# Optimization experiments

Hardware: AMD Instinct MI355X
Metric: run time of the kernel (lower is better)

The kernel has to match this reference:

```python
import jax, jax.numpy as jnp
import numpy as np

B, S, E = 4, 2048, 1024
H, Dh = 16, 64


def setup_inputs() -> dict:
    key = jax.random.key(0)
    ks = jax.random.split(key, 9)
    scale_in = 1.0 / np.sqrt(E)
    scale_out = 1.0 / np.sqrt(H * Dh)
    x = jax.random.normal(ks[0], (B, S, E), dtype=jnp.float32)
    # Per-head projection weights stacked over heads: [H, E, Dh]
    Wq = jax.random.uniform(ks[1], (H, E, Dh), jnp.float32, -scale_in, scale_in)
    bq = jax.random.uniform(ks[2], (H, Dh), jnp.float32, -scale_in, scale_in)
    Wk = jax.random.uniform(ks[3], (H, E, Dh), jnp.float32, -scale_in, scale_in)
    bk = jax.random.uniform(ks[4], (H, Dh), jnp.float32, -scale_in, scale_in)
    Wv = jax.random.uniform(ks[5], (H, E, Dh), jnp.float32, -scale_in, scale_in)
    bv = jax.random.uniform(ks[6], (H, Dh), jnp.float32, -scale_in, scale_in)
    # Output projection: [H*Dh, E]
    Wo = jax.random.uniform(ks[7], (H * Dh, E), jnp.float32, -scale_out, scale_out)
    bo = jax.random.uniform(ks[8], (E,), jnp.float32, -scale_out, scale_out)
    return {"x": x, "Wq": Wq, "bq": bq, "Wk": Wk, "bk": bk,
            "Wv": Wv, "bv": bv, "Wo": Wo, "bo": bo}


def reference(x, Wq, bq, Wk, bk, Wv, bv, Wo, bo):
    # Per-head linear projections, batched over heads: [B, H, S, Dh]
    q = jnp.einsum('bse,hed->bhsd', x, Wq) + bq[None, :, None, :]
    k = jnp.einsum('bse,hed->bhsd', x, Wk) + bk[None, :, None, :]
    v = jnp.einsum('bse,hed->bhsd', x, Wv) + bv[None, :, None, :]
    scale = 1.0 / jnp.sqrt(jnp.asarray(Dh, dtype=x.dtype))
    scores = jnp.einsum('bhsd,bhtd->bhst', q, k) * scale  # [B, H, S, S]
    weights = jax.nn.softmax(scores, axis=-1)
    z = jnp.einsum('bhst,bhtd->bhsd', weights, v)  # [B, H, S, Dh]
    # Concat heads in module order: [B, S, H*Dh]
    z = jnp.transpose(z, (0, 2, 1, 3)).reshape(B, S, H * Dh)
    return z @ Wo + bo
```

## Files before the change

### kernel.cpp

```cpp
#include <hip/hip_runtime.h>
#include <hip/hip_bf16.h>

#define B_  4
#define S_  2048
#define E_  1024
#define H_  16
#define DH_ 64
#define M_  (B_*S_)
#define HD_ (H_*DH_)

typedef unsigned short u16;
typedef __attribute__((ext_vector_type(8))) __bf16 bf16x8;
typedef __attribute__((ext_vector_type(4))) __bf16 bf16x4;
typedef __attribute__((ext_vector_type(4))) float  f32x4;

#if __has_builtin(__builtin_amdgcn_exp2f)
#define EXP2F __builtin_amdgcn_exp2f
#else
#define EXP2F __builtin_exp2f
#endif

#define QSCALE 0.18033688011112042f

__device__ __forceinline__ void g2l16(const void* g, void* l) {
  __builtin_amdgcn_global_load_lds(
      (const __attribute__((address_space(1))) void*)g,
      (__attribute__((address_space(3))) void*)l, 16, 0, 0);
}

__device__ __forceinline__ u16 f2bf(float f) {
  union { float f; unsigned u; } v; v.f = f;
  unsigned r = v.u + 0x7FFFu + ((v.u >> 16) & 1u);
  return (u16)(r >> 16);
}

__global__ __launch_bounds__(256) void cvt_x_kernel(const float* __restrict__ x,
                                                    u16* __restrict__ xb) {
  int i = blockIdx.x * 256 + threadIdx.x;
  float4 v = ((const float4*)x)[i];
  ushort4 o;
  o.x = f2bf(v.x); o.y = f2bf(v.y); o.z = f2bf(v.z); o.w = f2bf(v.w);
  ((ushort4*)xb)[i] = o;
}

__global__ __launch_bounds__(256) void pack_wqkv_kernel(
    const float* __restrict__ Wq, const float* __restrict__ Wk,
    const float* __restrict__ Wv, u16* __restrict__ wt) {
  __shared__ u16 tile[64][66];
  int p = blockIdx.z, h = blockIdx.y, e0 = blockIdx.x * 64;
  const float* src = (p == 0 ? Wq : (p == 1 ? Wk : Wv)) + h * (E_ * DH_);
  int tid = threadIdx.x;
#pragma unroll
  for (int r = 0; r < 16; ++r) {
    int idx = r * 256 + tid;
    int el = idx >> 6, d = idx & 63;
    tile[el][d] = f2bf(src[(e0 + el) * DH_ + d]);
  }
  __syncthreads();
  u16* dst = wt + (p * HD_ + h * DH_) * E_;
#pragma unroll
  for (int r = 0; r < 16; ++r) {
    int idx = r * 256 + tid;
    int d = idx >> 6, el = idx & 63;
    dst[d * E_ + e0 + el] = tile[el][d];
  }
}

__global__ __launch_bounds__(256) void pack_wo_kernel(const float* __restrict__ Wo,
                                                      u16* __restrict__ wt) {
  __shared__ u16 tile[64][66];
  int c0 = blockIdx.y * 64, e0 = blockIdx.x * 64;
  int tid = threadIdx.x;
#pragma unroll
  for (int r = 0; r < 16; ++r) {
    int idx = r * 256 + tid;
    int cl = idx >> 6, el = idx & 63;
    tile[cl][el] = f2bf(Wo[(c0 + cl) * E_ + e0 + el]);
  }
  __syncthreads();
#pragma unroll
  for (int r = 0; r < 16; ++r) {
    int idx = r * 256 + tid;
    int er = idx >> 6, cl = idx & 63;
    wt[(e0 + er) * HD_ + c0 + cl] = tile[cl][er];
  }
}

__global__ __launch_bounds__(256) void transpose_v_kernel(
    const u16* __restrict__ vin, u16* __restrict__ vout) {
  __shared__ u16 t[64][72];
  const int tid = threadIdx.x;
  const int bh = blockIdx.y, st = blockIdx.x * 64;
  const u16* src = vin + ((size_t)((bh >> 4) * S_ + st)) * HD_ + (bh & 15) * 64;
#pragma unroll
  for (int rr = 0; rr < 2; ++rr) {
    int idx = rr * 256 + tid;
    int s = idx >> 3, ch = idx & 7;
    *(uint4*)&t[s][ch * 8] = *(const uint4*)(src + s * HD_ + ch * 8);
  }
  __syncthreads();
  u16* dst = vout + ((size_t)bh) * DH_ * S_ + st;
#pragma unroll
  for (int rr = 0; rr < 2; ++rr) {
    int idx = rr * 256 + tid;
    int d = idx >> 3, sc = (idx & 7) * 8;
    ushort4 o0, o1;
    o0.x = t[sc + 0][d]; o0.y = t[sc + 1][d]; o0.z = t[sc + 2][d]; o0.w = t[sc + 3][d];
    o1.x = t[sc + 4][d]; o1.y = t[sc + 5][d]; o1.z = t[sc + 6][d]; o1.w = t[sc + 7][d];
    *(ushort4*)(dst + (size_t)d * S_ + sc) = o0;
    *(ushort4*)(dst + (size_t)d * S_ + sc + 4) = o1;
  }
}

template <int MODE>
__global__ __launch_bounds__(256) void gemm_bt_kernel(
    const u16* __restrict__ A, const u16* __restrict__ Bt,
    const float* __restrict__ b0, const float* __restrict__ b1,
    const float* __restrict__ b2,
    u16* __restrict__ oQ, u16* __restrict__ oK, u16* __restrict__ oV,
    float* __restrict__ oF) {
  constexpr int K = 1024;
  __shared__ __align__(16) u16 As[128 * 32];
  __shared__ __align__(16) u16 Bs[128 * 32];
  const int tid = threadIdx.x;
  const int lane = tid & 63, wv = tid >> 6;
  const int wm = (wv >> 1) * 64, wn = (wv & 1) * 64;
  const int q4 = lane >> 4, lm = lane & 15;
  const int tileM = blockIdx.y * 128, tileN = blockIdx.x * 128;

  const int c0 = tid, c1 = tid + 256;
  const u16* gA0 = A + (tileM + (c0 >> 2)) * K + (((c0 & 3) ^ ((c0 >> 2) & 3)) * 8);
  const u16* gA1 = A + (tileM + (c1 >> 2)) * K + (((c1 & 3) ^ ((c1 >> 2) & 3)) * 8);
  const u16* gB0 = Bt + (tileN + (c0 >> 2)) * K + (((c0 & 3) ^ ((c0 >> 2) & 3)) * 8);
  const u16* gB1 = Bt + (tileN + (c1 >> 2)) * K + (((c1 & 3) ^ ((c1 >> 2) & 3)) * 8);
  u16* lA0 = As + c0 * 8; u16* lA1 = As + c1 * 8;
  u16* lB0 = Bs + c0 * 8; u16* lB1 = Bs + c1 * 8;

  f32x4 acc[4][4] = {};

  int aoff[4], boff[4];
#pragma unroll
  for (int i = 0; i < 4; ++i) {
    int ra = wm + i * 16 + lm;
    aoff[i] = ra * 32 + ((q4 ^ (ra & 3)) * 8);
    int rb = wn + i * 16 + lm;
    boff[i] = rb * 32 + ((q4 ^ (rb & 3)) * 8);
  }

  for (int k0 = 0; k0 < K; k0 += 32) {
    g2l16(gA0 + k0, lA0);
    g2l16(gA1 + k0, lA1);
    g2l16(gB0 + k0, lB0);
    g2l16(gB1 + k0, lB1);
    __syncthreads();
    bf16x8 af[4], bf[4];
#pragma unroll
    for (int i = 0; i < 4; ++i) af[i] = *(const bf16x8*)(As + aoff[i]);
#pragma unroll
    for (int j = 0; j < 4; ++j) bf[j] = *(const bf16x8*)(Bs + boff[j]);
#pragma unroll
    for (int i = 0; i < 4; ++i)
#pragma unroll
      for (int j = 0; j < 4; ++j)
        acc[i][j] = __builtin_amdgcn_mfma_f32_16x16x32_bf16(af[i], bf[j], acc[i][j], 0, 0, 0);
    __syncthreads();
  }

#pragma unroll
  for (int j = 0; j < 4; ++j) {
    int n = tileN + wn + j * 16 + lm;
    float bs;
    int proj = 0, cc = n;
    if (MODE == 1) {
      bs = b0[n];
    } else {
      proj = n >> 10; cc = n & 1023;
      const float* bp = (proj == 0 ? b0 : (proj == 1 ? b1 : b2));
      bs = bp[cc];
    }
#pragma unroll
    for (int i = 0; i < 4; ++i) {
#pragma unroll
      for (int r = 0; r < 4; ++r) {
        int m = tileM + wm + i * 16 + q4 * 4 + r;
        float val = acc[i][j][r] + bs;
        if (MODE == 1) {
          oF[m * HD_ + n] = val;
        } else {
          u16* optr = (proj == 0 ? oQ : (proj == 1 ? oK : oV));
          float scl = (proj == 0 ? QSCALE : 1.0f);
          optr[m * 1024 + cc] = f2bf(val * scl);
        }
      }
    }
  }
}

__global__ __launch_bounds__(256, 2) void flash_kernel(
    const u16* __restrict__ Q, const u16* __restrict__ Kb,
    const u16* __restrict__ Vt, u16* __restrict__ Z) {
  __shared__ __align__(16) u16 Ks[2][64 * 64];
  __shared__ __align__(16) u16 Vs[2][64 * 64];
  const int tid = threadIdx.x, lane = tid & 63, wv = tid >> 6;
  const int q4 = lane >> 4, lm = lane & 15;

  const int bid = blockIdx.x;
  const int bh = bid >> 3, qt = bid & 7;
  const int b = bh >> 4, h = bh & 15;

  const u16* qbase = Q + ((size_t)(b * S_ + qt * 256)) * HD_ + h * DH_;
  const u16* kbase = Kb + (size_t)b * S_ * HD_ + h * DH_;
  const u16* vbase = Vt + ((size_t)(b * H_ + h)) * DH_ * S_;
  u16* zbase = Z + ((size_t)(b * S_ + qt * 256)) * HD_ + h * DH_;

  const int c0 = tid,       r0 = c0 >> 3, s0 = ((c0 & 7) ^ (r0 & 7)) * 8;
  const int c1 = tid + 256, r1 = c1 >> 3, s1 = ((c1 & 7) ^ (r1 & 7)) * 8;
  const int kr0 = ((r0 >> 4) & 1) * 32 + ((r0 >> 2) & 3) * 8 + (r0 >> 5) * 4 + (r0 & 3);
  const int kr1 = ((r1 >> 4) & 1) * 32 + ((r1 >> 2) & 3) * 8 + (r1 >> 5) * 4 + (r1 & 3);

  bf16x8 qf[4][2];
#pragma unroll
  for (int qs = 0; qs < 4; ++qs)
#pragma unroll
    for (int dc = 0; dc < 2; ++dc)
      qf[qs][dc] = *(const bf16x8*)(qbase + (wv * 64 + qs * 16 + lm) * HD_ + dc * 32 + q4 * 8);

  const bf16x8 ones = {(__bf16)1.f, (__bf16)1.f, (__bf16)1.f, (__bf16)1.f,
                       (__bf16)1.f, (__bf16)1.f, (__bf16)1.f, (__bf16)1.f};

  int koff[4][2], voff[2][4];
#pragma unroll
  for (int kb = 0; kb < 4; ++kb)
#pragma unroll
    for (int dc = 0; dc < 2; ++dc) {
      int row = kb * 16 + lm;
      koff[kb][dc] = row * 64 + (((dc * 4 + q4) ^ (row & 7)) * 8);
    }
#pragma unroll
  for (int ck = 0; ck < 2; ++ck)
#pragma unroll
    for (int db = 0; db < 4; ++db) {
      int row = db * 16 + lm;
      voff[ck][db] = row * 64 + (((ck * 4 + q4) ^ (row & 7)) * 8);
    }

  f32x4 oacc[4][4] = {};
  f32x4 liacc[4] = {};

  {
    g2l16(kbase + kr0 * HD_ + s0, Ks[0] + c0 * 8);
    g2l16(kbase + kr1 * HD_ + s1, Ks[0] + c1 * 8);
    g2l16(vbase + r0 * S_ + s0, Vs[0] + c0 * 8);
    g2l16(vbase + r1 * S_ + s1, Vs[0] + c1 * 8);
  }

  for (int t = 0; t < 32; ++t) {
    const int pb = t & 1;
    __syncthreads();
    if (t < 31) {
      const u16* kt = kbase + (size_t)(t + 1) * 64 * HD_;
      const u16* vt = vbase + (t + 1) * 64;
      g2l16(kt + kr0 * HD_ + s0, Ks[1 - pb] + c0 * 8);
      g2l16(kt + kr1 * HD_ + s1, Ks[1 - pb] + c1 * 8);
      g2l16(vt + r0 * S_ + s0, Vs[1 - pb] + c0 * 8);
      g2l16(vt + r1 * S_ + s1, Vs[1 - pb] + c1 * 8);
    }
    const u16* Kp = Ks[pb];
    const u16* Vp = Vs[pb];

#pragma unroll
    for (int ck = 0; ck < 2; ++ck) {
      bf16x8 ka0 = *(const bf16x8*)(Kp + koff[ck][0]);
      bf16x8 ka1 = *(const bf16x8*)(Kp + koff[ck][1]);
      bf16x8 kb0 = *(const bf16x8*)(Kp + koff[ck + 2][0]);
      bf16x8 kb1 = *(const bf16x8*)(Kp + koff[ck + 2][1]);
      bf16x8 pf[4];
#pragma unroll
      for (int qs = 0; qs < 4; ++qs) {
        f32x4 sa = {}, sb = {};
        sa = __builtin_amdgcn_mfma_f32_16x16x32_bf16(ka0, qf[qs][0], sa, 0, 0, 0);
        sa = __builtin_amdgcn_mfma_f32_16x16x32_bf16(ka1, qf[qs][1], sa, 0, 0, 0);
        sb = __builtin_amdgcn_mfma_f32_16x16x32_bf16(kb0, qf[qs][0], sb, 0, 0, 0);
        sb = __builtin_amdgcn_mfma_f32_16x16x32_bf16(kb1, qf[qs][1], sb, 0, 0, 0);
        f32x4 pa, pb2;
#pragma unroll
        for (int r = 0; r < 4; ++r) { pa[r] = EXP2F(sa[r]); pb2[r] = EXP2F(sb[r]); }
        bf16x4 la = __builtin_convertvector(pa, bf16x4);
        bf16x4 lb = __builtin_convertvector(pb2, bf16x4);
        pf[qs] = __builtin_shufflevector(la, lb, 0, 1, 2, 3, 4, 5, 6, 7);
      }
#pragma unroll
      for (int qs = 0; qs < 4; ++qs)
        liacc[qs] = __builtin_amdgcn_mfma_f32_16x16x32_bf16(pf[qs], ones, liacc[qs], 0, 0, 0);
#pragma unroll
      for (int db = 0; db < 4; ++db) {
        bf16x8 vf = *(const bf16x8*)(Vp + voff[ck][db]);
#pragma unroll
        for (int qs = 0; qs < 4; ++qs)
          oacc[qs][db] = __builtin_amdgcn_mfma_f32_16x16x32_bf16(pf[qs], vf, oacc[qs][db], 0, 0, 0);
      }
    }
  }

#pragma unroll
  for (int qs = 0; qs < 4; ++qs) {
    float rin[4];
#pragma unroll
    for (int r = 0; r < 4; ++r) rin[r] = 1.f / liacc[qs][r];
#pragma unroll
    for (int db = 0; db < 4; ++db)
#pragma unroll
      for (int r = 0; r < 4; ++r)
        zbase[(wv * 64 + qs * 16 + q4 * 4 + r) * HD_ + db * 16 + lm] =
            f2bf(oacc[qs][db][r] * rin[r]);
  }
}

extern "C" void kernel_launch(void* const* d_in, const int* in_sizes, int n_in,
                              void* d_out, int out_size, void* d_ws, size_t ws_size,
                              hipStream_t stream) {
  const float* x  = (const float*)d_in[0];
  const float* Wq = (const float*)d_in[1];
  const float* bq = (const float*)d_in[2];
  const float* Wk = (const float*)d_in[3];
  const float* bk = (const float*)d_in[4];
  const float* Wv = (const float*)d_in[5];
  const float* bv = (const float*)d_in[6];
  const float* Wo = (const float*)d_in[7];
  const float* bo = (const float*)d_in[8];
  float* out = (float*)d_out;

  char* w = (char*)d_ws;
  u16*   xb    = (u16*)w;   w += (size_t)M_ * E_ * 2;
  u16*   wqkvT = (u16*)w;   w += (size_t)3 * HD_ * E_ * 2;
  u16*   woT   = (u16*)w;   w += (size_t)E_ * HD_ * 2;
  u16*   qB    = (u16*)w;   w += (size_t)M_ * HD_ * 2;
  u16*   kB    = (u16*)w;   w += (size_t)M_ * HD_ * 2;
  u16*   vT    = (u16*)w;   w += (size_t)M_ * HD_ * 2;
  u16*   zB    = (u16*)w;   w += (size_t)M_ * HD_ * 2;
  u16*   vB    = zB;

  cvt_x_kernel<<<dim3(M_ * E_ / 4 / 256), 256, 0, stream>>>(x, xb);
  pack_wqkv_kernel<<<dim3(16, 16, 3), 256, 0, stream>>>(Wq, Wk, Wv, wqkvT);
  pack_wo_kernel<<<dim3(16, 16), 256, 0, stream>>>(Wo, woT);
  gemm_bt_kernel<0><<<dim3(24, 64), 256, 0, stream>>>(xb, wqkvT, bq, bk, bv,
                                                      qB, kB, vB, nullptr);
  transpose_v_kernel<<<dim3(32, 64), 256, 0, stream>>>(vB, vT);
  flash_kernel<<<dim3(512), 256, 0, stream>>>(qB, kB, vT, zB);
  gemm_bt_kernel<1><<<dim3(8, 64), 256, 0, stream>>>(zB, woT, bo, nullptr, nullptr,
                                                     nullptr, nullptr, nullptr, out);
}
```

Before: 284.1 us.

## Merge prep kernels, deepen GEMM K-tile to 64, use vector bf16 conversion in epilogues

Fuses the x conversion and the two weight-packing kernels into one launch that dispatches on block index, removing two kernel launches. The GEMM's K-tile grows from 32 to 64 with an 8-way XOR swizzle, halving the number of barrier pairs per tile at the cost of double the LDS footprint. The GEMM and flash epilogues replace the manual round-to-nearest bf16 conversion with a vector convertvector, though the stores are still scattered 16-bit writes.

```diff
diff --git a/kernel.cpp b/kernel.cpp
--- a/kernel.cpp
+++ b/kernel.cpp
@@ -34,55 +34,53 @@
   return (u16)(r >> 16);
 }
 
-__global__ __launch_bounds__(256) void cvt_x_kernel(const float* __restrict__ x,
-                                                    u16* __restrict__ xb) {
-  int i = blockIdx.x * 256 + threadIdx.x;
-  float4 v = ((const float4*)x)[i];
-  ushort4 o;
-  o.x = f2bf(v.x); o.y = f2bf(v.y); o.z = f2bf(v.z); o.w = f2bf(v.w);
-  ((ushort4*)xb)[i] = o;
-}
-
-__global__ __launch_bounds__(256) void pack_wqkv_kernel(
-    const float* __restrict__ Wq, const float* __restrict__ Wk,
-    const float* __restrict__ Wv, u16* __restrict__ wt) {
+__global__ __launch_bounds__(256) void prep_kernel(
+    const float* __restrict__ x, const float* __restrict__ Wq,
+    const float* __restrict__ Wk, const float* __restrict__ Wv,
+    const float* __restrict__ Wo,
+    u16* __restrict__ xb, u16* __restrict__ wqkvT, u16* __restrict__ woT) {
   __shared__ u16 tile[64][66];
-  int p = blockIdx.z, h = blockIdx.y, e0 = blockIdx.x * 64;
-  const float* src = (p == 0 ? Wq : (p == 1 ? Wk : Wv)) + h * (E_ * DH_);
-  int tid = threadIdx.x;
-#pragma unroll
-  for (int r = 0; r < 16; ++r) {
-    int idx = r * 256 + tid;
-    int el = idx >> 6, d = idx & 63;
-    tile[el][d] = f2bf(src[(e0 + el) * DH_ + d]);
-  }
-  __syncthreads();
-  u16* dst = wt + (p * HD_ + h * DH_) * E_;
-#pragma unroll
-  for (int r = 0; r < 16; ++r) {
-    int idx = r * 256 + tid;
-    int d = idx >> 6, el = idx & 63;
-    dst[d * E_ + e0 + el] = tile[el][d];
-  }
-}
-
-__global__ __launch_bounds__(256) void pack_wo_kernel(const float* __restrict__ Wo,
-                                                      u16* __restrict__ wt) {
-  __shared__ u16 tile[64][66];
-  int c0 = blockIdx.y * 64, e0 = blockIdx.x * 64;
-  int tid = threadIdx.x;
-#pragma unroll
-  for (int r = 0; r < 16; ++r) {
-    int idx = r * 256 + tid;
-    int cl = idx >> 6, el = idx & 63;
-    tile[cl][el] = f2bf(Wo[(c0 + cl) * E_ + e0 + el]);
-  }
-  __syncthreads();
-#pragma unroll
-  for (int r = 0; r < 16; ++r) {
-    int idx = r * 256 + tid;
-    int er = idx >> 6, cl = idx & 63;
-    wt[(e0 + er) * HD_ + c0 + cl] = tile[cl][er];
+  const int blk = blockIdx.x, tid = threadIdx.x;
+  if (blk < 8192) {
+    int i = blk * 256 + tid;
+    float4 v = ((const float4*)x)[i];
+    ushort4 o;
+    o.x = f2bf(v.x); o.y = f2bf(v.y); o.z = f2bf(v.z); o.w = f2bf(v.w);
+    ((ushort4*)xb)[i] = o;
+  } else if (blk < 8960) {
+    int b2 = blk - 8192;
+    int p = b2 >> 8, h = (b2 >> 4) & 15, e0 = (b2 & 15) * 64;
+    const float* src = (p == 0 ? Wq : (p == 1 ? Wk : Wv)) + h * (E_ * DH_);
+#pragma unroll
+    for (int r = 0; r < 16; ++r) {
+      int idx = r * 256 + tid;
+      int el = idx >> 6, d = idx & 63;
+      tile[el][d] = f2bf(src[(e0 + el) * DH_ + d]);
+    }
+    __syncthreads();
+    u16* dst = wqkvT + (p * HD_ + h * DH_) * E_;
+#pragma unroll
+    for (int r = 0; r < 16; ++r) {
+      int idx = r * 256 + tid;
+      int d = idx >> 6, el = idx & 63;
+      dst[d * E_ + e0 + el] = tile[el][d];
+    }
+  } else {
+    int b3 = blk - 8960;
+    int c0 = (b3 >> 4) * 64, e0 = (b3 & 15) * 64;
+#pragma unroll
+    for (int r = 0; r < 16; ++r) {
+      int idx = r * 256 + tid;
+      int cl = idx >> 6, el = idx & 63;
+      tile[cl][el] = f2bf(Wo[(c0 + cl) * E_ + e0 + el]);
+    }
+    __syncthreads();
+#pragma unroll
+    for (int r = 0; r < 16; ++r) {
+      int idx = r * 256 + tid;
+      int er = idx >> 6, cl = idx & 63;
+      woT[(e0 + er) * HD_ + c0 + cl] = tile[cl][er];
+    }
   }
 }
 
@@ -120,49 +118,59 @@
     u16* __restrict__ oQ, u16* __restrict__ oK, u16* __restrict__ oV,
     float* __restrict__ oF) {
   constexpr int K = 1024;
-  __shared__ __align__(16) u16 As[128 * 32];
-  __shared__ __align__(16) u16 Bs[128 * 32];
+  __shared__ __align__(16) u16 As[128 * 64];
+  __shared__ __align__(16) u16 Bs[128 * 64];
   const int tid = threadIdx.x;
   const int lane = tid & 63, wv = tid >> 6;
   const int wm = (wv >> 1) * 64, wn = (wv & 1) * 64;
   const int q4 = lane >> 4, lm = lane & 15;
   const int tileM = blockIdx.y * 128, tileN = blockIdx.x * 128;
 
-  const int c0 = tid, c1 = tid + 256;
-  const u16* gA0 = A + (tileM + (c0 >> 2)) * K + (((c0 & 3) ^ ((c0 >> 2) & 3)) * 8);
-  const u16* gA1 = A + (tileM + (c1 >> 2)) * K + (((c1 & 3) ^ ((c1 >> 2) & 3)) * 8);
-  const u16* gB0 = Bt + (tileN + (c0 >> 2)) * K + (((c0 & 3) ^ ((c0 >> 2) & 3)) * 8);
-  const u16* gB1 = Bt + (tileN + (c1 >> 2)) * K + (((c1 & 3) ^ ((c1 >> 2) & 3)) * 8);
-  u16* lA0 = As + c0 * 8; u16* lA1 = As + c1 * 8;
-  u16* lB0 = Bs + c0 * 8; u16* lB1 = Bs + c1 * 8;
+  const u16* gA[4]; const u16* gB[4]; u16* lA[4]; u16* lB[4];
+#pragma unroll
+  for (int rr = 0; rr < 4; ++rr) {
+    int c = rr * 256 + tid;
+    int r = c >> 3, sw = ((c & 7) ^ (r & 7)) * 8;
+    gA[rr] = A + (size_t)(tileM + r) * K + sw;
+    gB[rr] = Bt + (size_t)(tileN + r) * K + sw;
+    lA[rr] = As + c * 8;
+    lB[rr] = Bs + c * 8;
+  }
 
   f32x4 acc[4][4] = {};
 
-  int aoff[4], boff[4];
-#pragma unroll
-  for (int i = 0; i < 4; ++i) {
-    int ra = wm + i * 16 + lm;
-    aoff[i] = ra * 32 + ((q4 ^ (ra & 3)) * 8);
-    int rb = wn + i * 16 + lm;
-    boff[i] = rb * 32 + ((q4 ^ (rb & 3)) * 8);
-  }
-
-  for (int k0 = 0; k0 < K; k0 += 32) {
-    g2l16(gA0 + k0, lA0);
-    g2l16(gA1 + k0, lA1);
-    g2l16(gB0 + k0, lB0);
-    g2l16(gB1 + k0, lB1);
-    __syncthreads();
-    bf16x8 af[4], bf[4];
-#pragma unroll
-    for (int i = 0; i < 4; ++i) af[i] = *(const bf16x8*)(As + aoff[i]);
-#pragma unroll
-    for (int j = 0; j < 4; ++j) bf[j] = *(const bf16x8*)(Bs + boff[j]);
-#pragma unroll
-    for (int i = 0; i < 4; ++i)
-#pragma unroll
-      for (int j = 0; j < 4; ++j)
-        acc[i][j] = __builtin_amdgcn_mfma_f32_16x16x32_bf16(af[i], bf[j], acc[i][j], 0, 0, 0);
+  int aoff[2][4], boff[2][4];
+#pragma unroll
+  for (int ks = 0; ks < 2; ++ks) {
+#pragma unroll
+    for (int i = 0; i < 4; ++i) {
+      int ra = wm + i * 16 + lm;
+      aoff[ks][i] = ra * 64 + (((ks * 4 + q4) ^ (ra & 7)) * 8);
+      int rb = wn + i * 16 + lm;
+      boff[ks][i] = rb * 64 + (((ks * 4 + q4) ^ (rb & 7)) * 8);
+    }
+  }
+
+  for (int k0 = 0; k0 < K; k0 += 64) {
+#pragma unroll
+    for (int rr = 0; rr < 4; ++rr) {
+      g2l16(gA[rr] + k0, lA[rr]);
+      g2l16(gB[rr] + k0, lB[rr]);
+    }
+    __syncthreads();
+#pragma unroll
+    for (int ks = 0; ks < 2; ++ks) {
+      bf16x8 af[4], bf[4];
+#pragma unroll
+      for (int i = 0; i < 4; ++i) af[i] = *(const bf16x8*)(As + aoff[ks][i]);
+#pragma unroll
+      for (int j = 0; j < 4; ++j) bf[j] = *(const bf16x8*)(Bs + boff[ks][j]);
+#pragma unroll
+      for (int i = 0; i < 4; ++i)
+#pragma unroll
+        for (int j = 0; j < 4; ++j)
+          acc[i][j] = __builtin_amdgcn_mfma_f32_16x16x32_bf16(af[i], bf[j], acc[i][j], 0, 0, 0);
+    }
     __syncthreads();
   }
 
@@ -180,17 +188,22 @@
     }
 #pragma unroll
     for (int i = 0; i < 4; ++i) {
-#pragma unroll
-      for (int r = 0; r < 4; ++r) {
-        int m = tileM + wm + i * 16 + q4 * 4 + r;
-        float val = acc[i][j][r] + bs;
-        if (MODE == 1) {
-          oF[m * HD_ + n] = val;
-        } else {
-          u16* optr = (proj == 0 ? oQ : (proj == 1 ? oK : oV));
-          float scl = (proj == 0 ? QSCALE : 1.0f);
-          optr[m * 1024 + cc] = f2bf(val * scl);
-        }
+      int m0 = tileM + wm + i * 16 + q4 * 4;
+      if (MODE == 1) {
+#pragma unroll
+        for (int r = 0; r < 4; ++r) oF[(m0 + r) * HD_ + n] = acc[i][j][r] + bs;
+      } else {
+        u16* optr = (proj == 0 ? oQ : (proj == 1 ? oK : oV));
+        float scl = (proj == 0 ? QSCALE : 1.0f);
+        f32x4 vv;
+#pragma unroll
+        for (int r = 0; r < 4; ++r) vv[r] = (acc[i][j][r] + bs) * scl;
+        bf16x4 ov = __builtin_convertvector(vv, bf16x4);
+        ushort4 us = *(ushort4*)&ov;
+        optr[(m0 + 0) * 1024 + cc] = us.x;
+        optr[(m0 + 1) * 1024 + cc] = us.y;
+        optr[(m0 + 2) * 1024 + cc] = us.z;
+        optr[(m0 + 3) * 1024 + cc] = us.w;
       }
     }
   }
@@ -308,11 +321,18 @@
 #pragma unroll
     for (int r = 0; r < 4; ++r) rin[r] = 1.f / liacc[qs][r];
 #pragma unroll
-    for (int db = 0; db < 4; ++db)
-#pragma unroll
-      for (int r = 0; r < 4; ++r)
-        zbase[(wv * 64 + qs * 16 + q4 * 4 + r) * HD_ + db * 16 + lm] =
-            f2bf(oacc[qs][db][r] * rin[r]);
+    for (int db = 0; db < 4; ++db) {
+      f32x4 vv;
+#pragma unroll
+      for (int r = 0; r < 4; ++r) vv[r] = oacc[qs][db][r] * rin[r];
+      bf16x4 ov = __builtin_convertvector(vv, bf16x4);
+      ushort4 us = *(ushort4*)&ov;
+      int m0 = wv * 64 + qs * 16 + q4 * 4;
+      zbase[(m0 + 0) * HD_ + db * 16 + lm] = us.x;
+      zbase[(m0 + 1) * HD_ + db * 16 + lm] = us.y;
+      zbase[(m0 + 2) * HD_ + db * 16 + lm] = us.z;
+      zbase[(m0 + 3) * HD_ + db * 16 + lm] = us.w;
+    }
   }
 }
 
@@ -340,9 +360,7 @@
   u16*   zB    = (u16*)w;   w += (size_t)M_ * HD_ * 2;
   u16*   vB    = zB;
 
-  cvt_x_kernel<<<dim3(M_ * E_ / 4 / 256), 256, 0, stream>>>(x, xb);
-  pack_wqkv_kernel<<<dim3(16, 16, 3), 256, 0, stream>>>(Wq, Wk, Wv, wqkvT);
-  pack_wo_kernel<<<dim3(16, 16), 256, 0, stream>>>(Wo, woT);
+  prep_kernel<<<dim3(9216), 256, 0, stream>>>(x, Wq, Wk, Wv, Wo, xb, wqkvT, woT);
   gemm_bt_kernel<0><<<dim3(24, 64), 256, 0, stream>>>(xb, wqkvT, bq, bk, bv,
                                                       qB, kB, vB, nullptr);
   transpose_v_kernel<<<dim3(32, 64), 256, 0, stream>>>(vB, vT);
```

Result: faster. 266.5 us (-6.2%).
